# Kernel tuning notes

Hardware: AMD Instinct MI355X
Metric: run time of the kernel (lower is better)

The kernel has to match this reference:

```python
import jax, jax.numpy as jnp
import numpy as np
from jax import lax

PORTION = 0.1
IOU_TH = 0.25
C = 20  # VOC classes


def greedy_nms(iou_sub, thr):
    """Greedy NMS over candidates already sorted by descending score.
    iou_sub: (K,K) IoU map restricted to candidates. Returns (K,) bool keep mask.
    Matches instance_nms: pop highest score, drop all with iou >= thr."""
    K = iou_sub.shape[0]

    def body(i, state):
        alive, keep = state
        sel = alive[i]
        keep = keep.at[i].set(sel)
        suppress = iou_sub[i] >= thr
        alive = jnp.where(sel, alive & ~suppress, alive)
        return (alive, keep)

    alive0 = jnp.ones((K,), dtype=bool)
    keep0 = jnp.zeros((K,), dtype=bool)
    _, keep = lax.fori_loop(0, K, body, (alive0, keep0))
    return keep


def setup_inputs() -> dict:
    N = 6144
    key = jax.random.key(0)
    k1, k2, k3, k4, k5 = jax.random.split(key, 5)
    predict_cls = jax.random.uniform(k1, (N, C + 1), dtype=jnp.float32)
    predict_det = jax.random.uniform(k2, (N, C + 1), dtype=jnp.float32)
    rois = jax.random.uniform(k3, (N, 5), dtype=jnp.float32) * 512.0
    labels = jax.random.randint(k4, (C,), 0, 2, dtype=jnp.int32)
    labels = labels.at[0].set(1)  # guarantee at least one positive class
    u = jax.random.uniform(k5, (N, N), dtype=jnp.float32)
    iou_map = 0.5 * (u + u.T)  # symmetric, like a precomputed mask-IoU map
    iou_map = iou_map.at[jnp.arange(N), jnp.arange(N)].set(1.0)
    return {"predict_cls": predict_cls, "predict_det": predict_det,
            "rois": rois, "labels": labels, "iou_map": iou_map}


def reference(predict_cls, predict_det, rois, labels, iou_map):
    # forward(..., diffuse=False) -> mist_label path
    rois = rois[:, 1:]                      # strip batch-index column
    preds = predict_cls * predict_det       # (N, C+1)
    preds = preds[:, 1:]                    # drop background col -> (N, C)
    N = preds.shape[0]
    K = int(np.ceil(PORTION * N))           # keep_count

    gt_labels = jnp.zeros((N, C + 1), dtype=preds.dtype)
    gt_weights = -jnp.ones((N,), dtype=preds.dtype)

    # sequential per-class updates (order matters for gt_weights comparisons)
    for c in range(C):
        cls_prob = preds[:, c]
        order = jnp.argsort(-cls_prob)[:K]                       # top-K by score, descending
        sub = iou_map[order[:, None], order[None, :]]            # (K,K)
        keep = greedy_nms(sub, IOU_TH)                           # (K,) bool
        nms_mask = jnp.zeros((N,), dtype=bool).at[order].set(keep)
        upd = nms_mask & (cls_prob > gt_weights) & (labels[c] > 0)
        onehot = jax.nn.one_hot(c + 1, C + 1, dtype=preds.dtype)
        gt_labels = jnp.where(upd[:, None], onehot, gt_labels)
        gt_weights = jnp.where(upd, cls_prob, gt_weights)

    gt_idxs = jnp.sum(gt_labels, axis=-1) > 0                    # (N,) gt mask
    # overlaps = iou_map[:, gt_idxs], kept full-width with non-gt cols masked to -1
    overlaps = jnp.where(gt_idxs[None, :], iou_map, -1.0)
    max_v = jnp.max(overlaps, axis=-1)
    max_i = jnp.argmax(overlaps, axis=-1)

    pseudo_labels = gt_labels[max_i]                             # (N, C+1)
    loss_weights = gt_weights[max_i]                             # (N,)
    pseudo_iou_label = max_v

    ignore = max_v == 0
    pseudo_labels = jnp.where(ignore[:, None], 0.0, pseudo_labels)
    loss_weights = jnp.where(ignore, 0.0, loss_weights)
    bg = (max_v < IOU_TH) & ~ignore
    bg_onehot = jax.nn.one_hot(0, C + 1, dtype=preds.dtype)
    pseudo_labels = jnp.where(bg[:, None], bg_onehot, pseudo_labels)

    return pseudo_labels, pseudo_iou_label, loss_weights
```

## Files before the change

### kernel.cpp

```cpp
#include <hip/hip_runtime.h>
#include <hip/hip_bf16.h>
#include <stdint.h>

#define N_ROIS 6144
#define NCLS 20
#define TOPK 615
#define KPAD 640
#define IOU_TH 0.25f

#define BUCKETS 8192
#define CAND_CAP 1024
#define NWORDS 10

__global__ void k_preds(const float* __restrict__ pc, const float* __restrict__ pd,
                        float* __restrict__ preds_t) {
    int i = blockIdx.x * blockDim.x + threadIdx.x;
    if (i >= NCLS * N_ROIS) return;
    int c = i / N_ROIS, n = i - c * N_ROIS;
    int src = n * (NCLS + 1) + (c + 1);
    preds_t[i] = pc[src] * pd[src];
}

__global__ __launch_bounds__(1024) void k_topk(const float* __restrict__ preds_t,
                                               const int* __restrict__ labels,
                                               int* __restrict__ order) {
    int c = blockIdx.x;
    if (labels[c] <= 0) return;
    __shared__ int hist[BUCKETS];
    __shared__ unsigned long long cand[CAND_CAP];
    __shared__ int chunk[1024];
    __shared__ int thresh_bucket;
    __shared__ int cand_cnt;
    int tid = threadIdx.x;

    for (int i = tid; i < BUCKETS; i += 1024) hist[i] = 0;
    if (tid == 0) cand_cnt = 0;
    __syncthreads();

    float sc[6];
    #pragma unroll
    for (int k = 0; k < 6; ++k) {
        int n = tid + k * 1024;
        float s = preds_t[c * N_ROIS + n];
        sc[k] = s;
        int b = (int)(s * (float)BUCKETS);
        b = min(max(b, 0), BUCKETS - 1);
        atomicAdd(&hist[b], 1);
    }
    __syncthreads();

    int own = 0;
    #pragma unroll
    for (int k = 0; k < 8; ++k) own += hist[BUCKETS - 1 - (tid * 8 + k)];
    chunk[tid] = own;
    __syncthreads();
    for (int off = 1; off < 1024; off <<= 1) {
        int v = (tid >= off) ? chunk[tid - off] : 0;
        __syncthreads();
        chunk[tid] += v;
        __syncthreads();
    }
    int inc = chunk[tid];
    int exc = inc - own;
    if (exc < TOPK && inc >= TOPK) {
        int cum = exc;
        #pragma unroll
        for (int k = 0; k < 8; ++k) {
            int rb = tid * 8 + k;
            cum += hist[BUCKETS - 1 - rb];
            if (cum >= TOPK) { thresh_bucket = BUCKETS - 1 - rb; break; }
        }
    }
    __syncthreads();
    int tb = thresh_bucket;

    #pragma unroll
    for (int k = 0; k < 6; ++k) {
        int n = tid + k * 1024;
        float s = sc[k];
        int b = (int)(s * (float)BUCKETS);
        b = min(max(b, 0), BUCKETS - 1);
        if (b >= tb) {
            int pos = atomicAdd(&cand_cnt, 1);
            if (pos < CAND_CAP) {
                unsigned bits = __float_as_uint(s);
                cand[pos] = ((unsigned long long)(~bits) << 32) | (unsigned)n;
            }
        }
    }
    __syncthreads();
    int cc = min(cand_cnt, CAND_CAP);
    for (int i = tid; i < CAND_CAP; i += 1024)
        if (i >= cc) cand[i] = ~0ull;
    __syncthreads();

    for (unsigned k2 = 2; k2 <= CAND_CAP; k2 <<= 1) {
        for (unsigned j = k2 >> 1; j > 0; j >>= 1) {
            unsigned i = (unsigned)tid;
            unsigned ixj = i ^ j;
            if (ixj > i) {
                unsigned long long a = cand[i], b = cand[ixj];
                bool up = ((i & k2) == 0);
                if ((a > b) == up) { cand[i] = b; cand[ixj] = a; }
            }
            __syncthreads();
        }
    }
    if (tid < TOPK) order[c * KPAD + tid] = (int)(cand[tid] & 0xFFFFFFFFu);
}

__global__ __launch_bounds__(64) void k_nms(const float* __restrict__ iou,
                                            const int* __restrict__ labels,
                                            const int* __restrict__ order,
                                            unsigned char* __restrict__ kept) {
    int c = blockIdx.x;
    if (labels[c] <= 0) return;
    __shared__ int order_s[TOPK];
    __shared__ unsigned long long alive[NWORDS];
    int lane = threadIdx.x;
    for (int j = lane; j < TOPK; j += 64) order_s[j] = order[c * KPAD + j];
    if (lane < NWORDS) {
        unsigned long long m = ~0ull;
        if (lane == NWORDS - 1) m = (1ull << (TOPK - 64 * (NWORDS - 1))) - 1;
        alive[lane] = m;
    }
    __syncthreads();

    int i = 0;
    while (true) {
        int next = -1;
        for (int w = i >> 6; w < NWORDS; ++w) {
            unsigned long long m = alive[w];
            if (w == (i >> 6)) m &= (~0ull) << (i & 63);
            if (m) { next = w * 64 + __builtin_ctzll(m); break; }
        }
        if (next < 0) break;
        i = next;
        int bi = order_s[i];
        const float* row = iou + (size_t)bi * N_ROIS;
        #pragma unroll
        for (int k = 0; k < NWORDS; ++k) {
            unsigned long long w = alive[k];
            int j = k * 64 + lane;
            bool sup = false;
            if ((w >> lane) & 1ull)
                sup = row[order_s[j]] >= IOU_TH;
            unsigned long long bal = __ballot(sup);
            if (lane == 0) alive[k] = w & ~bal;
        }
        if (lane == 0) kept[c * N_ROIS + bi] = 1;
        __syncthreads();
    }
}

__global__ void k_assign(const float* __restrict__ preds_t, const int* __restrict__ labels,
                         const unsigned char* __restrict__ kept,
                         int* __restrict__ lab, float* __restrict__ wgt,
                         int* __restrict__ gtlist, int* __restrict__ gtcount) {
    int n = blockIdx.x * blockDim.x + threadIdx.x;
    if (n >= N_ROIS) return;
    float w = -1.0f; int l = 0;
    for (int c = 0; c < NCLS; ++c) {
        if (labels[c] > 0 && kept[c * N_ROIS + n]) {
            float p = preds_t[c * N_ROIS + n];
            if (p > w) { w = p; l = c + 1; }
        }
    }
    lab[n] = l; wgt[n] = w;
    if (l > 0) {
        int pos = atomicAdd(gtcount, 1);
        gtlist[pos] = n;
    }
}

__global__ void k_final(const float* __restrict__ iou, const int* __restrict__ lab,
                        const float* __restrict__ wgt, const int* __restrict__ gtlist,
                        const int* __restrict__ gtcount, float* __restrict__ out) {
    int n = blockIdx.x * blockDim.x + threadIdx.x;
    if (n >= N_ROIS) return;
    int J = *gtcount;
    float maxv; int maxi;
    if (J == 0) { maxv = -1.0f; maxi = 0; }
    else {
        maxv = -2.0f; maxi = N_ROIS;
        for (int t = 0; t < J; ++t) {
            int j = gtlist[t];
            float v = iou[(size_t)j * N_ROIS + n];
            if (v > maxv || (v == maxv && j < maxi)) { maxv = v; maxi = j; }
        }
    }
    float lw = wgt[maxi];
    int pl = lab[maxi];
    bool ignore = (maxv == 0.0f);
    bool bg = (maxv < IOU_TH) && !ignore;
    float row[NCLS + 1];
    #pragma unroll
    for (int k = 0; k <= NCLS; ++k) row[k] = 0.0f;
    if (ignore) { lw = 0.0f; }
    else if (bg) { row[0] = 1.0f; }
    else if (pl > 0) { row[pl] = 1.0f; }
    #pragma unroll
    for (int k = 0; k <= NCLS; ++k) out[(size_t)n * (NCLS + 1) + k] = row[k];
    out[(size_t)N_ROIS * (NCLS + 1) + n] = maxv;
    out[(size_t)N_ROIS * (NCLS + 1) + N_ROIS + n] = lw;
}

extern "C" void kernel_launch(void* const* d_in, const int* in_sizes, int n_in,
                              void* d_out, int out_size, void* d_ws, size_t ws_size,
                              hipStream_t stream) {
    const float* pc     = (const float*)d_in[0];
    const float* pd     = (const float*)d_in[1];
    const int*   labels = (const int*)d_in[3];
    const float* iou    = (const float*)d_in[4];
    float* out = (float*)d_out;

    char* ws = (char*)d_ws;
    size_t off = 0;
    float* preds_t = (float*)(ws + off);          off += (size_t)NCLS * N_ROIS * 4;
    int*   order   = (int*)(ws + off);            off += (size_t)NCLS * KPAD * 4;
    unsigned char* kept = (unsigned char*)(ws + off); off += (size_t)NCLS * N_ROIS;
    int*   gtcount = (int*)(ws + off);            off += 4;
    int*   lab     = (int*)(ws + off);            off += (size_t)N_ROIS * 4;
    float* wgt     = (float*)(ws + off);          off += (size_t)N_ROIS * 4;
    int*   gtlist  = (int*)(ws + off);            off += (size_t)N_ROIS * 4;

    hipMemsetAsync(kept, 0, (size_t)NCLS * N_ROIS + 4, stream);

    k_preds <<<(NCLS * N_ROIS + 255) / 256, 256, 0, stream>>>(pc, pd, preds_t);
    k_topk  <<<NCLS, 1024, 0, stream>>>(preds_t, labels, order);
    k_nms   <<<NCLS, 64, 0, stream>>>(iou, labels, order, kept);
    k_assign<<<(N_ROIS + 255) / 256, 256, 0, stream>>>(preds_t, labels, kept, lab, wgt, gtlist, gtcount);
    k_final <<<(N_ROIS + 255) / 256, 256, 0, stream>>>(iou, lab, wgt, gtlist, gtcount, out);
}
```

Measured before the change: 250.4 us.

## Fuse preds, top-k and NMS into one kernel with sparse kept-pair output

Replaces the five-kernel pipeline with two kernels. The first computes scores inline, picks the exact top-K by histogram plus in-bucket ranking in place of a bitonic sort, and runs NMS with 1024 threads using repeated block-wide argmin over the remaining candidates. It writes a compact list of kept (roi, score) pairs per class. The second kernel resolves cross-class winners in shared memory and computes per-roi max IoU over the gt list, removing the memset, the preds_t buffer, the dense kept map and the gtlist atomics. The risks are fixed caps (KEEP_CAP 256, EMAX 1024) that could drop entries, and a per-step block-wide reduction with two barriers for every kept box.

```diff
diff --git a/kernel.cpp b/kernel.cpp
--- a/kernel.cpp
+++ b/kernel.cpp
@@ -1,234 +1,229 @@
 #include <hip/hip_runtime.h>
-#include <hip/hip_bf16.h>
 #include <stdint.h>
 
 #define N_ROIS 6144
 #define NCLS 20
+#define NC1 21
 #define TOPK 615
-#define KPAD 640
 #define IOU_TH 0.25f
-
 #define BUCKETS 8192
-#define CAND_CAP 1024
-#define NWORDS 10
-
-__global__ void k_preds(const float* __restrict__ pc, const float* __restrict__ pd,
-                        float* __restrict__ preds_t) {
-    int i = blockIdx.x * blockDim.x + threadIdx.x;
-    if (i >= NCLS * N_ROIS) return;
-    int c = i / N_ROIS, n = i - c * N_ROIS;
-    int src = n * (NCLS + 1) + (c + 1);
-    preds_t[i] = pc[src] * pd[src];
+#define CAND 1024
+#define KEEP_CAP 256
+#define EMAX 1024
+
+__global__ __launch_bounds__(1024) void k_select_nms(
+    const float* __restrict__ pc, const float* __restrict__ pd,
+    const int* __restrict__ labels, const float* __restrict__ iou,
+    int* __restrict__ kept_cnt, int2* __restrict__ kept_pairs) {
+  const int c = blockIdx.x;
+  if (labels[c] <= 0) return;
+  __shared__ int hist[BUCKETS];
+  __shared__ unsigned long long key[CAND];
+  __shared__ int chunk[1024];
+  __shared__ int wsum[16];
+  __shared__ unsigned long long wmin[16];
+  __shared__ unsigned long long s_win;
+  __shared__ int s_tb, s_need, s_cnt, s_kcnt;
+  const int tid = threadIdx.x;
+
+  for (int i = tid; i < BUCKETS; i += 1024) hist[i] = 0;
+  key[tid] = ~0ull;
+  if (tid == 0) { s_cnt = 0; s_kcnt = 0; }
+  __syncthreads();
+
+  float sc[6];
+  #pragma unroll
+  for (int k = 0; k < 6; ++k) {
+    int n = tid + (k << 10);
+    int off = n * NC1 + (c + 1);
+    float s = pc[off] * pd[off];
+    sc[k] = s;
+    int b = (int)(s * (float)BUCKETS);
+    b = min(max(b, 0), BUCKETS - 1);
+    atomicAdd(&hist[b], 1);
+  }
+  __syncthreads();
+
+  int own = 0;
+  #pragma unroll
+  for (int k = 0; k < 8; ++k) own += hist[BUCKETS - 1 - (tid * 8 + k)];
+  chunk[tid] = own;
+  int r = own;
+  #pragma unroll
+  for (int m = 1; m < 64; m <<= 1) r += __shfl_xor(r, m, 64);
+  if ((tid & 63) == 0) wsum[tid >> 6] = r;
+  __syncthreads();
+
+  if (tid == 0) {
+    int cum = 0, w = 0;
+    for (; w < 15; ++w) { if (cum + wsum[w] >= TOPK) break; cum += wsum[w]; }
+    int t = w << 6;
+    for (;; ++t) { if (cum + chunk[t] >= TOPK) break; cum += chunk[t]; }
+    int tb = 0, need = TOPK - cum;
+    #pragma unroll
+    for (int k = 0; k < 8; ++k) {
+      int b = BUCKETS - 1 - (t * 8 + k);
+      int h = hist[b];
+      if (cum + h >= TOPK) { tb = b; need = TOPK - cum; break; }
+      cum += h;
+    }
+    s_tb = tb; s_need = need;
+  }
+  __syncthreads();
+  const int tb = s_tb, need = s_need;
+
+  #pragma unroll
+  for (int k = 0; k < 6; ++k) {
+    float s = sc[k];
+    int b = (int)(s * (float)BUCKETS);
+    b = min(max(b, 0), BUCKETS - 1);
+    if (b >= tb) {
+      int pos = atomicAdd(&s_cnt, 1);
+      if (pos < CAND) {
+        unsigned bits = __float_as_uint(s);
+        key[pos] = ((unsigned long long)(~bits) << 32) | (unsigned)(tid + (k << 10));
+      }
+    }
+  }
+  __syncthreads();
+
+  const int cnt = min(s_cnt, CAND);
+  {
+    unsigned long long mykey = key[tid];
+    bool demote = false;
+    if (tid < cnt && mykey != ~0ull) {
+      unsigned bits = ~(unsigned)(mykey >> 32);
+      float s = __uint_as_float(bits);
+      int b = (int)(s * (float)BUCKETS);
+      b = min(max(b, 0), BUCKETS - 1);
+      if (b == tb) {
+        int rank = 0;
+        for (int j = 0; j < cnt; ++j) {
+          unsigned long long kj = key[j];
+          if (kj < mykey) {
+            unsigned bj = ~(unsigned)(kj >> 32);
+            float sj = __uint_as_float(bj);
+            int bb = (int)(sj * (float)BUCKETS);
+            bb = min(max(bb, 0), BUCKETS - 1);
+            if (bb == tb) ++rank;
+          }
+        }
+        demote = (rank >= need);
+      }
+    }
+    __syncthreads();
+    if (demote) key[tid] = ~0ull;
+    __syncthreads();
+  }
+
+  while (true) {
+    unsigned long long v = key[tid];
+    #pragma unroll
+    for (int m = 1; m < 64; m <<= 1) {
+      unsigned lo = __shfl_xor((unsigned)v, m, 64);
+      unsigned hi = __shfl_xor((unsigned)(v >> 32), m, 64);
+      unsigned long long u = ((unsigned long long)hi << 32) | lo;
+      if (u < v) v = u;
+    }
+    if ((tid & 63) == 0) wmin[tid >> 6] = v;
+    __syncthreads();
+    if (tid == 0) {
+      unsigned long long m2 = wmin[0];
+      #pragma unroll
+      for (int w = 1; w < 16; ++w) if (wmin[w] < m2) m2 = wmin[w];
+      s_win = m2;
+    }
+    __syncthreads();
+    const unsigned long long win = s_win;
+    if (win == ~0ull) break;
+    const int bi = (int)(win & 0xffffffffu);
+    if (key[tid] == win) {
+      int p = s_kcnt;
+      if (p < KEEP_CAP)
+        kept_pairs[c * KEEP_CAP + p] = make_int2(bi, (int)(~(unsigned)(win >> 32)));
+      s_kcnt = p + 1;
+    }
+    if (key[tid] != ~0ull) {
+      int n = (int)(key[tid] & 0xffffffffu);
+      if (iou[(size_t)bi * N_ROIS + n] >= IOU_TH) key[tid] = ~0ull;
+    }
+    __syncthreads();
+  }
+  if (tid == 0) kept_cnt[c] = min(s_kcnt, KEEP_CAP);
 }
 
-__global__ __launch_bounds__(1024) void k_topk(const float* __restrict__ preds_t,
-                                               const int* __restrict__ labels,
-                                               int* __restrict__ order) {
-    int c = blockIdx.x;
-    if (labels[c] <= 0) return;
-    __shared__ int hist[BUCKETS];
-    __shared__ unsigned long long cand[CAND_CAP];
-    __shared__ int chunk[1024];
-    __shared__ int thresh_bucket;
-    __shared__ int cand_cnt;
-    int tid = threadIdx.x;
-
-    for (int i = tid; i < BUCKETS; i += 1024) hist[i] = 0;
-    if (tid == 0) cand_cnt = 0;
-    __syncthreads();
-
-    float sc[6];
-    #pragma unroll
-    for (int k = 0; k < 6; ++k) {
-        int n = tid + k * 1024;
-        float s = preds_t[c * N_ROIS + n];
-        sc[k] = s;
-        int b = (int)(s * (float)BUCKETS);
-        b = min(max(b, 0), BUCKETS - 1);
-        atomicAdd(&hist[b], 1);
-    }
-    __syncthreads();
-
-    int own = 0;
-    #pragma unroll
-    for (int k = 0; k < 8; ++k) own += hist[BUCKETS - 1 - (tid * 8 + k)];
-    chunk[tid] = own;
-    __syncthreads();
-    for (int off = 1; off < 1024; off <<= 1) {
-        int v = (tid >= off) ? chunk[tid - off] : 0;
-        __syncthreads();
-        chunk[tid] += v;
-        __syncthreads();
-    }
-    int inc = chunk[tid];
-    int exc = inc - own;
-    if (exc < TOPK && inc >= TOPK) {
-        int cum = exc;
-        #pragma unroll
-        for (int k = 0; k < 8; ++k) {
-            int rb = tid * 8 + k;
-            cum += hist[BUCKETS - 1 - rb];
-            if (cum >= TOPK) { thresh_bucket = BUCKETS - 1 - rb; break; }
-        }
-    }
-    __syncthreads();
-    int tb = thresh_bucket;
-
-    #pragma unroll
-    for (int k = 0; k < 6; ++k) {
-        int n = tid + k * 1024;
-        float s = sc[k];
-        int b = (int)(s * (float)BUCKETS);
-        b = min(max(b, 0), BUCKETS - 1);
-        if (b >= tb) {
-            int pos = atomicAdd(&cand_cnt, 1);
-            if (pos < CAND_CAP) {
-                unsigned bits = __float_as_uint(s);
-                cand[pos] = ((unsigned long long)(~bits) << 32) | (unsigned)n;
-            }
-        }
-    }
-    __syncthreads();
-    int cc = min(cand_cnt, CAND_CAP);
-    for (int i = tid; i < CAND_CAP; i += 1024)
-        if (i >= cc) cand[i] = ~0ull;
-    __syncthreads();
-
-    for (unsigned k2 = 2; k2 <= CAND_CAP; k2 <<= 1) {
-        for (unsigned j = k2 >> 1; j > 0; j >>= 1) {
-            unsigned i = (unsigned)tid;
-            unsigned ixj = i ^ j;
-            if (ixj > i) {
-                unsigned long long a = cand[i], b = cand[ixj];
-                bool up = ((i & k2) == 0);
-                if ((a > b) == up) { cand[i] = b; cand[ixj] = a; }
-            }
-            __syncthreads();
-        }
-    }
-    if (tid < TOPK) order[c * KPAD + tid] = (int)(cand[tid] & 0xFFFFFFFFu);
-}
-
-__global__ __launch_bounds__(64) void k_nms(const float* __restrict__ iou,
-                                            const int* __restrict__ labels,
-                                            const int* __restrict__ order,
-                                            unsigned char* __restrict__ kept) {
-    int c = blockIdx.x;
-    if (labels[c] <= 0) return;
-    __shared__ int order_s[TOPK];
-    __shared__ unsigned long long alive[NWORDS];
-    int lane = threadIdx.x;
-    for (int j = lane; j < TOPK; j += 64) order_s[j] = order[c * KPAD + j];
-    if (lane < NWORDS) {
-        unsigned long long m = ~0ull;
-        if (lane == NWORDS - 1) m = (1ull << (TOPK - 64 * (NWORDS - 1))) - 1;
-        alive[lane] = m;
-    }
-    __syncthreads();
-
-    int i = 0;
-    while (true) {
-        int next = -1;
-        for (int w = i >> 6; w < NWORDS; ++w) {
-            unsigned long long m = alive[w];
-            if (w == (i >> 6)) m &= (~0ull) << (i & 63);
-            if (m) { next = w * 64 + __builtin_ctzll(m); break; }
-        }
-        if (next < 0) break;
-        i = next;
-        int bi = order_s[i];
-        const float* row = iou + (size_t)bi * N_ROIS;
-        #pragma unroll
-        for (int k = 0; k < NWORDS; ++k) {
-            unsigned long long w = alive[k];
-            int j = k * 64 + lane;
-            bool sup = false;
-            if ((w >> lane) & 1ull)
-                sup = row[order_s[j]] >= IOU_TH;
-            unsigned long long bal = __ballot(sup);
-            if (lane == 0) alive[k] = w & ~bal;
-        }
-        if (lane == 0) kept[c * N_ROIS + bi] = 1;
-        __syncthreads();
-    }
-}
-
-__global__ void k_assign(const float* __restrict__ preds_t, const int* __restrict__ labels,
-                         const unsigned char* __restrict__ kept,
-                         int* __restrict__ lab, float* __restrict__ wgt,
-                         int* __restrict__ gtlist, int* __restrict__ gtcount) {
-    int n = blockIdx.x * blockDim.x + threadIdx.x;
-    if (n >= N_ROIS) return;
-    float w = -1.0f; int l = 0;
-    for (int c = 0; c < NCLS; ++c) {
-        if (labels[c] > 0 && kept[c * N_ROIS + n]) {
-            float p = preds_t[c * N_ROIS + n];
-            if (p > w) { w = p; l = c + 1; }
-        }
-    }
-    lab[n] = l; wgt[n] = w;
-    if (l > 0) {
-        int pos = atomicAdd(gtcount, 1);
-        gtlist[pos] = n;
-    }
-}
-
-__global__ void k_final(const float* __restrict__ iou, const int* __restrict__ lab,
-                        const float* __restrict__ wgt, const int* __restrict__ gtlist,
-                        const int* __restrict__ gtcount, float* __restrict__ out) {
-    int n = blockIdx.x * blockDim.x + threadIdx.x;
-    if (n >= N_ROIS) return;
-    int J = *gtcount;
-    float maxv; int maxi;
-    if (J == 0) { maxv = -1.0f; maxi = 0; }
-    else {
-        maxv = -2.0f; maxi = N_ROIS;
-        for (int t = 0; t < J; ++t) {
-            int j = gtlist[t];
-            float v = iou[(size_t)j * N_ROIS + n];
-            if (v > maxv || (v == maxv && j < maxi)) { maxv = v; maxi = j; }
-        }
-    }
-    float lw = wgt[maxi];
-    int pl = lab[maxi];
-    bool ignore = (maxv == 0.0f);
-    bool bg = (maxv < IOU_TH) && !ignore;
-    float row[NCLS + 1];
-    #pragma unroll
-    for (int k = 0; k <= NCLS; ++k) row[k] = 0.0f;
-    if (ignore) { lw = 0.0f; }
-    else if (bg) { row[0] = 1.0f; }
-    else if (pl > 0) { row[pl] = 1.0f; }
-    #pragma unroll
-    for (int k = 0; k <= NCLS; ++k) out[(size_t)n * (NCLS + 1) + k] = row[k];
-    out[(size_t)N_ROIS * (NCLS + 1) + n] = maxv;
-    out[(size_t)N_ROIS * (NCLS + 1) + N_ROIS + n] = lw;
+__global__ __launch_bounds__(256) void k_out(
+    const float* __restrict__ iou, const int* __restrict__ labels,
+    const int* __restrict__ kept_cnt, const int2* __restrict__ kept_pairs,
+    float* __restrict__ out) {
+  __shared__ int   e_n[EMAX];
+  __shared__ float e_s[EMAX];
+  __shared__ short e_c[EMAX];
+  __shared__ unsigned char e_ok[EMAX];
+  __shared__ int s_E;
+  const int tid = threadIdx.x;
+  if (tid == 0) s_E = 0;
+  __syncthreads();
+  if (tid < NCLS && labels[tid] > 0) {
+    int cnt = min(kept_cnt[tid], KEEP_CAP);
+    for (int t = 0; t < cnt; ++t) {
+      int2 pr = kept_pairs[tid * KEEP_CAP + t];
+      int p = atomicAdd(&s_E, 1);
+      if (p < EMAX) { e_n[p] = pr.x; e_s[p] = __int_as_float(pr.y); e_c[p] = (short)tid; }
+    }
+  }
+  __syncthreads();
+  const int E = min(s_E, EMAX);
+  for (int i = tid; i < E; i += 256) {
+    int n = e_n[i]; float s = e_s[i]; int cc = e_c[i];
+    bool ok = true;
+    for (int j = 0; j < E; ++j) {
+      if (j == i || e_n[j] != n) continue;
+      float sj = e_s[j];
+      if (sj > s || (sj == s && e_c[j] < cc)) { ok = false; break; }
+    }
+    e_ok[i] = ok ? 1 : 0;
+  }
+  __syncthreads();
+
+  const int n = blockIdx.x * 256 + tid;
+  float maxv = -1.0f;
+  int mslot = -1, mn = N_ROIS;
+  for (int j = 0; j < E; ++j) {
+    if (!e_ok[j]) continue;
+    int nj = e_n[j];
+    float v = iou[(size_t)nj * N_ROIS + n];
+    if (v > maxv || (v == maxv && nj < mn)) { maxv = v; mn = nj; mslot = j; }
+  }
+  float lw; int pl;
+  if (mslot >= 0) { lw = e_s[mslot]; pl = (int)e_c[mslot] + 1; }
+  else { lw = -1.0f; pl = 0; }
+  bool ignore = (maxv == 0.0f);
+  bool bg = (maxv < IOU_TH) && !ignore;
+  float row[NC1];
+  #pragma unroll
+  for (int k = 0; k < NC1; ++k) row[k] = 0.0f;
+  if (ignore) lw = 0.0f;
+  else if (bg) row[0] = 1.0f;
+  else row[pl] = 1.0f;
+  #pragma unroll
+  for (int k = 0; k < NC1; ++k) out[(size_t)n * NC1 + k] = row[k];
+  out[(size_t)N_ROIS * NC1 + n] = maxv;
+  out[(size_t)N_ROIS * NC1 + N_ROIS + n] = lw;
 }
 
 extern "C" void kernel_launch(void* const* d_in, const int* in_sizes, int n_in,
                               void* d_out, int out_size, void* d_ws, size_t ws_size,
                               hipStream_t stream) {
-    const float* pc     = (const float*)d_in[0];
-    const float* pd     = (const float*)d_in[1];
-    const int*   labels = (const int*)d_in[3];
-    const float* iou    = (const float*)d_in[4];
-    float* out = (float*)d_out;
-
-    char* ws = (char*)d_ws;
-    size_t off = 0;
-    float* preds_t = (float*)(ws + off);          off += (size_t)NCLS * N_ROIS * 4;
-    int*   order   = (int*)(ws + off);            off += (size_t)NCLS * KPAD * 4;
-    unsigned char* kept = (unsigned char*)(ws + off); off += (size_t)NCLS * N_ROIS;
-    int*   gtcount = (int*)(ws + off);            off += 4;
-    int*   lab     = (int*)(ws + off);            off += (size_t)N_ROIS * 4;
-    float* wgt     = (float*)(ws + off);          off += (size_t)N_ROIS * 4;
-    int*   gtlist  = (int*)(ws + off);            off += (size_t)N_ROIS * 4;
-
-    hipMemsetAsync(kept, 0, (size_t)NCLS * N_ROIS + 4, stream);
-
-    k_preds <<<(NCLS * N_ROIS + 255) / 256, 256, 0, stream>>>(pc, pd, preds_t);
-    k_topk  <<<NCLS, 1024, 0, stream>>>(preds_t, labels, order);
-    k_nms   <<<NCLS, 64, 0, stream>>>(iou, labels, order, kept);
-    k_assign<<<(N_ROIS + 255) / 256, 256, 0, stream>>>(preds_t, labels, kept, lab, wgt, gtlist, gtcount);
-    k_final <<<(N_ROIS + 255) / 256, 256, 0, stream>>>(iou, lab, wgt, gtlist, gtcount, out);
+  const float* pc     = (const float*)d_in[0];
+  const float* pd     = (const float*)d_in[1];
+  const int*   labels = (const int*)d_in[3];
+  const float* iou    = (const float*)d_in[4];
+  float* out = (float*)d_out;
+
+  int2* kept_pairs = (int2*)d_ws;
+  int*  kept_cnt   = (int*)((char*)d_ws + NCLS * KEEP_CAP * 8);
+
+  k_select_nms<<<NCLS, 1024, 0, stream>>>(pc, pd, labels, iou, kept_cnt, kept_pairs);
+  k_out<<<N_ROIS / 256, 256, 0, stream>>>(iou, labels, kept_cnt, kept_pairs, out);
 }
```

Measured after the change: 281.5 us. 12.4% more time.
